# Kernel tuning notes

Hardware: AMD Instinct MI355X
Metric: run time of the kernel (lower is better)

The kernel has to match this reference:

```python
import jax, jax.numpy as jnp
import numpy as np
import math

B, L = 16, 60            # batch, max labels per image
NC, NA = 80, 3           # classes, anchors
NH, NW = 76, 76          # grid
N_CH = 5 + NC
ANCHORS = [1.25, 1.625, 2.0, 3.75, 4.125, 2.875]  # grid units (w,h pairs)
ANCH_MASK = [0, 1, 2]
IGNORE_THRE = 0.5
EPS = 1e-16


def pairwise_iou(a, b, xyxy=True, ciou=False):
    """a: [N,4], b: [M,4] -> [N,M]; mirrors ciou_yolov4 (incl. its xyxy quirks)."""
    if xyxy:
        tl = jnp.maximum(a[:, None, :2], b[None, :, :2])
        br = jnp.minimum(a[:, None, 2:], b[None, :, 2:])
        con_tl = jnp.minimum(a[:, None, :2], b[None, :, :2])
        con_br = jnp.maximum(a[:, None, 2:], b[None, :, 2:])
        rho2 = ((a[:, None, 0] + a[:, None, 2] - b[None, :, 0] - b[None, :, 2]) ** 2
                + (a[:, None, 1] + a[:, None, 3] - b[None, :, 1] - b[None, :, 3]) ** 2) / 4.0
        w1 = a[:, 2] - a[:, 0]; h1 = a[:, 3] - a[:, 1]
        w2 = b[:, 2] - b[:, 0]; h2 = b[:, 3] - b[:, 1]
        area_a = w1 * h1
        area_b = w2 * h2
    else:
        tl = jnp.maximum(a[:, None, :2] - a[:, None, 2:] / 2, b[None, :, :2] - b[None, :, 2:] / 2)
        br = jnp.minimum(a[:, None, :2] + a[:, None, 2:] / 2, b[None, :, :2] + b[None, :, 2:] / 2)
        con_tl = jnp.minimum(a[:, None, :2] - a[:, None, 2:] / 2, b[None, :, :2] - b[None, :, 2:] / 2)
        con_br = jnp.maximum(a[:, None, :2] + a[:, None, 2:] / 2, b[None, :, :2] + b[None, :, 2:] / 2)
        rho2 = (((a[:, None, :2] - b[None, :, :2]) ** 2) / 4.0).sum(-1)
        w1 = a[:, 2]; h1 = a[:, 3]; w2 = b[:, 2]; h2 = b[:, 3]
        area_a = a[:, 2] * a[:, 3]
        area_b = b[:, 2] * b[:, 3]
    en = jnp.prod((tl < br).astype(a.dtype), axis=2)
    area_i = jnp.prod(br - tl, axis=2) * en
    area_u = area_a[:, None] + area_b[None, :] - area_i
    iou = area_i / jnp.maximum(area_u, EPS)  # eps only guards all-zero padded boxes
    if ciou:
        c2 = ((con_br - con_tl) ** 2).sum(-1) + EPS
        v = (4.0 / math.pi ** 2) * (jnp.arctan(w1 / jnp.maximum(h1, EPS))[:, None]
                                    - jnp.arctan(w2 / jnp.maximum(h2, EPS))[None, :]) ** 2
        alpha = jax.lax.stop_gradient(v / jnp.maximum(1.0 - iou + v, EPS))
        return iou - (rho2 / c2 + v * alpha)
    return iou


def _clip_log(x):
    # torch BCE clamps log at -100
    return jnp.maximum(jnp.log(x), -100.0)


def bce_sum(p, t, w=None):
    el = -(t * _clip_log(p) + (1.0 - t) * _clip_log(1.0 - p))
    if w is not None:
        el = el * w
    return el.sum()


def build_targets(pred, labels):
    f32 = pred.dtype
    aw = jnp.asarray(ANCHORS[0:-1:2], f32)  # [NA]
    ah = jnp.asarray(ANCHORS[1::2], f32)
    n_valid = (labels.sum(2) > 0).sum(1)                     # [B]
    valid = jnp.arange(L)[None, :] < n_valid[:, None]        # [B,L]
    tx = labels[:, :, 1] * NW
    ty = labels[:, :, 2] * NH
    tw = labels[:, :, 3] * NW
    th = labels[:, :, 4] * NH
    ti = tx.astype(jnp.int32)  # truncation == floor for positive coords
    tj = ty.astype(jnp.int32)
    # anchor matching: boxes [0,0,w,h] treated as xyxy, CIoU (as in the original)
    ref_anchors = jnp.zeros((NA, 4), f32).at[:, 2].set(aw).at[:, 3].set(ah)
    zeros = jnp.zeros_like(tw)
    tb_wh = jnp.stack([zeros, zeros, tw, th], axis=-1)       # [B,L,4]
    anch_ious = jax.vmap(lambda t: pairwise_iou(t, ref_anchors, xyxy=True, ciou=True))(tb_wh)
    best_n_all = jnp.argmax(anch_ious, axis=-1)              # [B,L]
    best_n = best_n_all % 3
    best_mask = jnp.zeros_like(valid)
    for m in ANCH_MASK:
        best_mask = best_mask | (best_n_all == m)
    sel = valid & best_mask                                  # labels that get assigned
    # ignore mask from pred-vs-truth IoU (xywh, plain IoU)
    tb = jnp.stack([tx, ty, tw, th], axis=-1)                # [B,L,4]
    pious = jax.vmap(lambda p, t: pairwise_iou(p, t, xyxy=False, ciou=False))(
        pred.reshape(B, -1, 4), tb)                          # [B,NA*NH*NW,L]
    pious = jnp.where(valid[:, None, :], pious, -jnp.inf)
    best_iou = pious.max(axis=-1).reshape(B, NA, NH, NW)
    any_sel = sel.any(axis=1)                                # original 'continue' semantics
    obj_mask = jnp.where(any_sel[:, None, None, None],
                         (best_iou <= IGNORE_THRE).astype(f32),
                         jnp.ones((), f32))
    # scatter assignments; a_idx = NA (out of bounds) => dropped
    a_idx = jnp.where(sel, best_n, NA)
    b_idx = jnp.broadcast_to(jnp.arange(B)[:, None], (B, L))
    obj_mask = obj_mask.at[b_idx, a_idx, tj, ti].set(1.0, mode='drop')
    dx = tx - jnp.floor(tx)
    dy = ty - jnp.floor(ty)
    lw = jnp.log(tw / aw[best_n] + EPS)
    lh = jnp.log(th / ah[best_n] + EPS)
    onehot = jax.nn.one_hot(labels[:, :, 0].astype(jnp.int32), NC, dtype=f32)
    tvec = jnp.concatenate([dx[..., None], dy[..., None], lw[..., None], lh[..., None],
                            jnp.ones((B, L, 1), f32), onehot], axis=-1)  # [B,L,N_CH]
    target = jnp.zeros((B, NA, NH, NW, N_CH), f32).at[b_idx, a_idx, tj, ti].set(tvec, mode='drop')
    tgt_mask = jnp.zeros((B, NA, NH, NW, 4 + NC), f32).at[b_idx, a_idx, tj, ti].set(1.0, mode='drop')
    scale = jnp.sqrt(2.0 - tw * th / float(NW * NH))
    tgt_scale = jnp.zeros((B, NA, NH, NW, 2), f32).at[b_idx, a_idx, tj, ti].set(
        jnp.broadcast_to(scale[..., None], (B, L, 2)), mode='drop')
    return obj_mask, tgt_mask, tgt_scale, target


def setup_inputs() -> dict:
    key = jax.random.key(0)
    k1, k2, k3, k4 = jax.random.split(key, 4)
    output = jax.random.normal(k1, (B, NA * N_CH, NH, NW), jnp.float32)
    cls = jax.random.randint(k2, (B, L), 0, NC).astype(jnp.float32)
    xy = jax.random.uniform(k3, (B, L, 2), minval=0.02, maxval=0.98)
    wh = jax.random.uniform(k4, (B, L, 2), minval=0.02, maxval=0.5)
    target = jnp.concatenate([cls[..., None], xy, wh], axis=-1)  # [B,L,5] cls,cx,cy,w,h in [0,1]
    return {"output": output, "target": target}


def reference(output, target):
    labels = jax.lax.stop_gradient(target)
    out = output.reshape(B, NA, N_CH, NH, NW).transpose(0, 1, 3, 4, 2)  # [B,NA,NH,NW,N_CH]
    out = jnp.concatenate([jax.nn.sigmoid(out[..., :2]), out[..., 2:4],
                           jax.nn.sigmoid(out[..., 4:])], axis=-1)
    gx = jnp.arange(NW, dtype=out.dtype)
    gy = jnp.arange(NH, dtype=out.dtype)
    aw = jnp.asarray(ANCHORS[0:-1:2], out.dtype)
    ah = jnp.asarray(ANCHORS[1::2], out.dtype)
    px = out[..., 0] + gx[None, None, None, :]
    py = out[..., 1] + gy[None, None, :, None]
    pw = jnp.exp(out[..., 2]) * aw[None, :, None, None]
    ph = jnp.exp(out[..., 3]) * ah[None, :, None, None]
    pred = jax.lax.stop_gradient(jnp.stack([px, py, pw, ph], axis=-1))  # pred.data in torch
    obj_mask, tgt_mask, tgt_scale, tgt = build_targets(pred, labels)
    oxy = out[..., 0:2] * tgt_mask[..., 0:2]
    owh = out[..., 2:4] * tgt_mask[..., 2:4] * tgt_scale
    oobj = out[..., 4] * obj_mask
    ocls = out[..., 5:] * tgt_mask[..., 4:]
    txy = tgt[..., 0:2] * tgt_mask[..., 0:2]
    twh = tgt[..., 2:4] * tgt_mask[..., 2:4] * tgt_scale
    tobj = tgt[..., 4] * obj_mask
    tcls = tgt[..., 5:] * tgt_mask[..., 4:]
    loss_xy = bce_sum(oxy, txy, w=tgt_scale * tgt_scale)
    loss_wh = ((owh - twh) ** 2).sum() / 2.0
    loss_obj = bce_sum(oobj, tobj)
    loss_cls = bce_sum(ocls, tcls)
    return (loss_xy + loss_wh + loss_obj + loss_cls) / B
```

## Files before the change

### kernel.cpp

```cpp
#include <hip/hip_runtime.h>
#include <math.h>

namespace {

constexpr int kB = 16, kL = 60, kNC = 80, kNA = 3, kNH = 76, kNW = 76, kNCH = 85;
constexpr int kPlane = kNH * kNW;
constexpr int kCellsPerB = kNA * kPlane;
constexpr int kBX = (kCellsPerB + 255) / 256;
constexpr int kNPart = kB * kBX;
constexpr float kEps = 1e-16f;

__device__ float g_partials[kNPart];

__device__ __forceinline__ float sigm(float x) { return 1.0f / (1.0f + expf(-x)); }
__device__ __forceinline__ float softplus(float x) {
  return fmaxf(x, 0.0f) + log1pf(expf(-fabsf(x)));
}
__device__ __forceinline__ float anchW(int a) { return a == 0 ? 1.25f : (a == 1 ? 2.0f : 4.125f); }
__device__ __forceinline__ float anchH(int a) { return a == 0 ? 1.625f : (a == 1 ? 3.75f : 2.875f); }

__global__ __launch_bounds__(256) void main_loss(const float* __restrict__ out,
                                                 const float* __restrict__ labels) {
  const int b = blockIdx.y;
  const int tid = threadIdx.x;
  __shared__ float st[kL][12];
  __shared__ int snv;

  if (tid < 64) {
    const int l = tid;
    const bool in = l < kL;
    float c0 = 0.f, x = 0.f, y = 0.f, w = 0.f, h = 0.f;
    if (in) {
      const float* p = labels + ((size_t)b * kL + l) * 5;
      c0 = p[0]; x = p[1]; y = p[2]; w = p[3]; h = p[4];
    }
    const unsigned long long m = __ballot(in && (c0 + x + y + w + h > 0.0f));
    const int nv = __popcll(m);
    if (l == 0) snv = nv;
    if (in) {
      const bool valid = l < nv;
      const float tx = x * (float)kNW, ty = y * (float)kNH;
      const float tw = w * (float)kNW, th = h * (float)kNH;
      const int ti = (int)tx, tj = (int)ty;

      const float at0 = atanf(tw / fmaxf(th, kEps));
      float best = -INFINITY;
      int bn = 0;
#pragma unroll
      for (int k = 0; k < kNA; ++k) {
        const float aw = anchW(k), ah = anchH(k);
        const float miw = fminf(tw, aw), mih = fminf(th, ah);
        const float en = ((0.0f < miw) && (0.0f < mih)) ? 1.0f : 0.0f;
        const float ai = miw * mih * en;
        const float au = tw * th + aw * ah - ai;
        const float iou = ai / fmaxf(au, kEps);
        const float dw = tw - aw, dh = th - ah;
        const float rho2 = (dw * dw + dh * dh) * 0.25f;
        const float mw = fmaxf(tw, aw), mh = fmaxf(th, ah);
        const float c2 = mw * mw + mh * mh + kEps;
        const float da = at0 - atanf(aw / ah);
        const float v = (4.0f / (float)(M_PI * M_PI)) * da * da;
        const float alpha = v / fmaxf(1.0f - iou + v, kEps);
        const float ciou = iou - (rho2 / c2 + v * alpha);
        if (ciou > best) { best = ciou; bn = k; }
      }
      st[l][0] = tx - tw * 0.5f; st[l][1] = ty - th * 0.5f;
      st[l][2] = tx + tw * 0.5f; st[l][3] = ty + th * 0.5f;
      st[l][4] = tw * th;
      st[l][5] = __int_as_float(valid ? ((bn * kNH + tj) * kNW + ti) : -1);
      st[l][6] = tx - floorf(tx);
      st[l][7] = ty - floorf(ty);
      st[l][8] = logf(tw / anchW(bn) + kEps);
      st[l][9] = logf(th / anchH(bn) + kEps);
      st[l][10] = sqrtf(2.0f - tw * th * (1.0f / (float)(kNW * kNH)));
      st[l][11] = __int_as_float((int)c0);
    }
  }
  __syncthreads();

  float acc = 0.0f;
  const int c = blockIdx.x * 256 + tid;
  int winner = -1;
  if (c < kCellsPerB) {
    const unsigned a = (unsigned)c / (unsigned)kPlane;
    const unsigned r = (unsigned)c - a * (unsigned)kPlane;
    const unsigned j = r / (unsigned)kNW;
    const unsigned i = r - j * (unsigned)kNW;
    const float* base = out + ((size_t)(b * kNA + (int)a) * kNCH) * kPlane + r;
    const float x0 = base[0];
    const float x1 = base[(size_t)kPlane];
    const float x2 = base[(size_t)2 * kPlane];
    const float x3 = base[(size_t)3 * kPlane];
    const float x4 = base[(size_t)4 * kPlane];

    const float px = sigm(x0) + (float)i;
    const float py = sigm(x1) + (float)j;
    const float pw = expf(x2) * anchW((int)a);
    const float ph = expf(x3) * anchH((int)a);
    const float px1 = px - 0.5f * pw, px2 = px + 0.5f * pw;
    const float py1 = py - 0.5f * ph, py2 = py + 0.5f * ph;
    const float ap = pw * ph;

    bool flag = false;
    const int nv = snv;
#pragma unroll 4
    for (int t = 0; t < nv; ++t) {
      const float4 bx = *reinterpret_cast<const float4*>(&st[t][0]);
      const float2 ak = *reinterpret_cast<const float2*>(&st[t][4]);
      const float tlx = fmaxf(px1, bx.x), tly = fmaxf(py1, bx.y);
      const float brx = fminf(px2, bx.z), bry = fminf(py2, bx.w);
      const bool ok = (tlx < brx) && (tly < bry);
      const float ai = ok ? (brx - tlx) * (bry - tly) : 0.0f;
      const float au = ap + ak.x - ai;
      flag = flag || (ai + ai > au);
      if (__float_as_int(ak.y) == c) winner = t;
    }

    const float sp4 = softplus(x4);
    if (winner >= 0) {
      acc += sp4 - x4;
      const float sc = st[winner][10];
      const float w2 = sc * sc;
      acc += (softplus(x0) - st[winner][6] * x0 + softplus(x1) - st[winner][7] * x1) * w2;
      const float d2 = x2 - st[winner][8], d3 = x3 - st[winner][9];
      acc += 0.5f * w2 * (d2 * d2 + d3 * d3);
    } else if (!flag) {
      acc += sp4;
    }
  }

  {
    const int lane = tid & 63;
    unsigned long long pend = __ballot(winner >= 0);
    while (pend) {
      const int src = (int)(__ffsll(pend) - 1);
      pend &= pend - 1;
      const int wc = __shfl(c, src);
      const int wt = __shfl(winner, src);
      const int cls = __float_as_int(st[wt][11]);
      const unsigned wa = (unsigned)wc / (unsigned)kPlane;
      const unsigned wr = (unsigned)wc - wa * (unsigned)kPlane;
      const float* wb = out + ((size_t)(b * kNA + (int)wa) * kNCH + 5) * kPlane + wr;
      const float v0 = wb[(size_t)lane * kPlane];
      float s = softplus(v0) - (lane == cls ? v0 : 0.0f);
      if (lane < kNC - 64) {
        const float v1 = wb[(size_t)(lane + 64) * kPlane];
        s += softplus(v1) - (lane + 64 == cls ? v1 : 0.0f);
      }
#pragma unroll
      for (int off = 32; off > 0; off >>= 1) s += __shfl_down(s, off);
      if (lane == 0) acc += s;
    }
  }

#pragma unroll
  for (int off = 32; off > 0; off >>= 1) acc += __shfl_down(acc, off);
  __shared__ float sred[4];
  if ((tid & 63) == 0) sred[tid >> 6] = acc;
  __syncthreads();
  if (tid == 0) g_partials[b * kBX + blockIdx.x] = sred[0] + sred[1] + sred[2] + sred[3];
}

__global__ void finalize(float* __restrict__ outp) {
  const int tid = threadIdx.x;
  double acc = 0.0;
  for (int idx = tid; idx < kNPart; idx += 256) acc += (double)g_partials[idx];
  __shared__ double s[256];
  s[tid] = acc;
  __syncthreads();
  for (int off = 128; off > 0; off >>= 1) {
    if (tid < off) s[tid] += s[tid + off];
    __syncthreads();
  }
  if (tid == 0) outp[0] = (float)(s[0] / (double)kB);
}

}

extern "C" void kernel_launch(void* const* d_in, const int* in_sizes, int n_in,
                              void* d_out, int out_size, void* d_ws, size_t ws_size,
                              hipStream_t stream) {
  const float* output = (const float*)d_in[0];
  const float* target = (const float*)d_in[1];
  float* outp = (float*)d_out;
  (void)d_ws; (void)ws_size;

  main_loss<<<dim3(kBX, kB), 256, 0, stream>>>(output, target);
  finalize<<<1, 256, 0, stream>>>(outp);
}
```

Measured before the change: 138.6 us.

## Process four cells per thread with float4 loads and shared label loop

Each thread now handles four consecutive grid cells, loading the five head channels as float4 vectors and amortizing each label's shared-memory read across four IoU tests. This cuts the thread count and the LDS traffic in the ignore-mask loop, and widens global loads. In exchange, register pressure rises and there are fewer blocks, which reduces parallelism for this small grid.

New measurement: 153.3 us. 10.6% more time.

```diff
diff --git a/kernel.cpp b/kernel.cpp
--- a/kernel.cpp
+++ b/kernel.cpp
@@ -5,8 +5,9 @@
 
 constexpr int kB = 16, kL = 60, kNC = 80, kNA = 3, kNH = 76, kNW = 76, kNCH = 85;
 constexpr int kPlane = kNH * kNW;
-constexpr int kCellsPerB = kNA * kPlane;
-constexpr int kBX = (kCellsPerB + 255) / 256;
+constexpr int kQuadsPerPlane = kPlane / 4;
+constexpr int kQuadsPerB = kNA * kQuadsPerPlane;
+constexpr int kBX = (kQuadsPerB + 255) / 256;
 constexpr int kNPart = kB * kBX;
 constexpr float kEps = 1e-16f;
 
@@ -42,7 +43,6 @@
       const float tx = x * (float)kNW, ty = y * (float)kNH;
       const float tw = w * (float)kNW, th = h * (float)kNH;
       const int ti = (int)tx, tj = (int)ty;
-
       const float at0 = atanf(tw / fmaxf(th, kEps));
       float best = -INFINITY;
       int bn = 0;
@@ -78,65 +78,80 @@
   }
   __syncthreads();
 
+  const int qid = blockIdx.x * 256 + tid;
+  const bool active = qid < kQuadsPerB;
+  int a = 0, r4 = 0;
+  if (active) { a = qid / kQuadsPerPlane; r4 = (qid - a * kQuadsPerPlane) * 4; }
+  const int cbase = a * kPlane + r4;
+
+  float xc[5][4];
+  float px1[4], px2[4], py1[4], py2[4], ap[4];
+  int winner[4] = {-1, -1, -1, -1};
+  unsigned flags = 0;
   float acc = 0.0f;
-  const int c = blockIdx.x * 256 + tid;
-  int winner = -1;
-  if (c < kCellsPerB) {
-    const unsigned a = (unsigned)c / (unsigned)kPlane;
-    const unsigned r = (unsigned)c - a * (unsigned)kPlane;
-    const unsigned j = r / (unsigned)kNW;
-    const unsigned i = r - j * (unsigned)kNW;
-    const float* base = out + ((size_t)(b * kNA + (int)a) * kNCH) * kPlane + r;
-    const float x0 = base[0];
-    const float x1 = base[(size_t)kPlane];
-    const float x2 = base[(size_t)2 * kPlane];
-    const float x3 = base[(size_t)3 * kPlane];
-    const float x4 = base[(size_t)4 * kPlane];
-
-    const float px = sigm(x0) + (float)i;
-    const float py = sigm(x1) + (float)j;
-    const float pw = expf(x2) * anchW((int)a);
-    const float ph = expf(x3) * anchH((int)a);
-    const float px1 = px - 0.5f * pw, px2 = px + 0.5f * pw;
-    const float py1 = py - 0.5f * ph, py2 = py + 0.5f * ph;
-    const float ap = pw * ph;
-
-    bool flag = false;
+
+  if (active) {
+    const float* base = out + ((size_t)(b * kNA + a) * kNCH) * kPlane + r4;
+#pragma unroll
+    for (int ch = 0; ch < 5; ++ch) {
+      const float4 v = *reinterpret_cast<const float4*>(base + (size_t)ch * kPlane);
+      xc[ch][0] = v.x; xc[ch][1] = v.y; xc[ch][2] = v.z; xc[ch][3] = v.w;
+    }
+    const float aw = anchW(a), ah = anchH(a);
+#pragma unroll
+    for (int k = 0; k < 4; ++k) {
+      const int r = r4 + k;
+      const int j = r / kNW, i = r - j * kNW;
+      const float px = sigm(xc[0][k]) + (float)i;
+      const float py = sigm(xc[1][k]) + (float)j;
+      const float pw = expf(xc[2][k]) * aw;
+      const float ph = expf(xc[3][k]) * ah;
+      px1[k] = px - 0.5f * pw; px2[k] = px + 0.5f * pw;
+      py1[k] = py - 0.5f * ph; py2[k] = py + 0.5f * ph;
+      ap[k] = pw * ph;
+    }
     const int nv = snv;
 #pragma unroll 4
     for (int t = 0; t < nv; ++t) {
       const float4 bx = *reinterpret_cast<const float4*>(&st[t][0]);
       const float2 ak = *reinterpret_cast<const float2*>(&st[t][4]);
-      const float tlx = fmaxf(px1, bx.x), tly = fmaxf(py1, bx.y);
-      const float brx = fminf(px2, bx.z), bry = fminf(py2, bx.w);
-      const bool ok = (tlx < brx) && (tly < bry);
-      const float ai = ok ? (brx - tlx) * (bry - tly) : 0.0f;
-      const float au = ap + ak.x - ai;
-      flag = flag || (ai + ai > au);
-      if (__float_as_int(ak.y) == c) winner = t;
-    }
-
-    const float sp4 = softplus(x4);
-    if (winner >= 0) {
-      acc += sp4 - x4;
-      const float sc = st[winner][10];
-      const float w2 = sc * sc;
-      acc += (softplus(x0) - st[winner][6] * x0 + softplus(x1) - st[winner][7] * x1) * w2;
-      const float d2 = x2 - st[winner][8], d3 = x3 - st[winner][9];
-      acc += 0.5f * w2 * (d2 * d2 + d3 * d3);
-    } else if (!flag) {
-      acc += sp4;
-    }
-  }
-
-  {
-    const int lane = tid & 63;
-    unsigned long long pend = __ballot(winner >= 0);
+      const int key = __float_as_int(ak.y);
+#pragma unroll
+      for (int k = 0; k < 4; ++k) {
+        const float tlx = fmaxf(px1[k], bx.x), tly = fmaxf(py1[k], bx.y);
+        const float brx = fminf(px2[k], bx.z), bry = fminf(py2[k], bx.w);
+        const bool ok = (tlx < brx) && (tly < bry);
+        const float ai = ok ? (brx - tlx) * (bry - tly) : 0.0f;
+        if (ai + ai > ap[k] + ak.x - ai) flags |= (1u << k);
+        if (key == cbase + k) winner[k] = t;
+      }
+    }
+#pragma unroll
+    for (int k = 0; k < 4; ++k) {
+      const float sp4 = softplus(xc[4][k]);
+      if (winner[k] >= 0) {
+        acc += sp4 - xc[4][k];
+        const float sc = st[winner[k]][10];
+        const float w2 = sc * sc;
+        acc += (softplus(xc[0][k]) - st[winner[k]][6] * xc[0][k] +
+                softplus(xc[1][k]) - st[winner[k]][7] * xc[1][k]) * w2;
+        const float d2 = xc[2][k] - st[winner[k]][8], d3 = xc[3][k] - st[winner[k]][9];
+        acc += 0.5f * w2 * (d2 * d2 + d3 * d3);
+      } else if (!((flags >> k) & 1u)) {
+        acc += sp4;
+      }
+    }
+  }
+
+  const int lane = tid & 63;
+#pragma unroll
+  for (int k = 0; k < 4; ++k) {
+    unsigned long long pend = __ballot(winner[k] >= 0);
     while (pend) {
       const int src = (int)(__ffsll(pend) - 1);
       pend &= pend - 1;
-      const int wc = __shfl(c, src);
-      const int wt = __shfl(winner, src);
+      const int wc = __shfl(cbase + k, src);
+      const int wt = __shfl(winner[k], src);
       const int cls = __float_as_int(st[wt][11]);
       const unsigned wa = (unsigned)wc / (unsigned)kPlane;
       const unsigned wr = (unsigned)wc - wa * (unsigned)kPlane;
```

## Precompute per-label target data in a separate kernel and read from global

Applied to the files above, without the earlier changes.

Label preprocessing (best-anchor CIoU selection, box corners, regression targets) moves from every main_loss block into a small prep kernel that runs once per batch image. Results go to global arrays that the main kernel reads through uniform loads. This removes redundant per-block label work and the block-wide barrier before the cell loop, so cell loads can start right away. The cost is an extra kernel launch and global or cache reads of box data in the inner loop instead of LDS reads.

New measurement: 143.1 us. 3.2% more time.

```diff
diff --git a/kernel.cpp b/kernel.cpp
--- a/kernel.cpp
+++ b/kernel.cpp
@@ -10,6 +10,12 @@
 constexpr int kNPart = kB * kBX;
 constexpr float kEps = 1e-16f;
 
+struct __align__(32) BoxT { float x1, y1, x2, y2, area; int key; int p0, p1; };
+struct __align__(32) RegT { float dx, dy, lw, lh, sc; int cls; int p0, p1; };
+
+__device__ BoxT g_boxes[kB][kL];
+__device__ RegT g_regr[kB][kL];
+__device__ int g_nv[kB];
 __device__ float g_partials[kNPart];
 
 __device__ __forceinline__ float sigm(float x) { return 1.0f / (1.0f + expf(-x)); }
@@ -19,110 +25,118 @@
 __device__ __forceinline__ float anchW(int a) { return a == 0 ? 1.25f : (a == 1 ? 2.0f : 4.125f); }
 __device__ __forceinline__ float anchH(int a) { return a == 0 ? 1.625f : (a == 1 ? 3.75f : 2.875f); }
 
+__global__ void prep_labels(const float* __restrict__ labels) {
+  const int b = blockIdx.x;
+  const int l = threadIdx.x;
+  const bool in = l < kL;
+  float c0 = 0.f, x = 0.f, y = 0.f, w = 0.f, h = 0.f;
+  if (in) {
+    const float* p = labels + ((size_t)b * kL + l) * 5;
+    c0 = p[0]; x = p[1]; y = p[2]; w = p[3]; h = p[4];
+  }
+  const unsigned long long m = __ballot(in && (c0 + x + y + w + h > 0.0f));
+  const int nv = __popcll(m);
+  if (l == 0) g_nv[b] = nv;
+  if (!in) return;
+  const bool valid = l < nv;
+
+  const float tx = x * (float)kNW, ty = y * (float)kNH;
+  const float tw = w * (float)kNW, th = h * (float)kNH;
+  const int ti = (int)tx, tj = (int)ty;
+
+  const float at0 = atanf(tw / fmaxf(th, kEps));
+  float best = -INFINITY;
+  int bn = 0;
+#pragma unroll
+  for (int k = 0; k < kNA; ++k) {
+    const float aw = anchW(k), ah = anchH(k);
+    const float miw = fminf(tw, aw), mih = fminf(th, ah);
+    const float en = ((0.0f < miw) && (0.0f < mih)) ? 1.0f : 0.0f;
+    const float ai = miw * mih * en;
+    const float au = tw * th + aw * ah - ai;
+    const float iou = ai / fmaxf(au, kEps);
+    const float dw = tw - aw, dh = th - ah;
+    const float rho2 = (dw * dw + dh * dh) * 0.25f;
+    const float mw = fmaxf(tw, aw), mh = fmaxf(th, ah);
+    const float c2 = mw * mw + mh * mh + kEps;
+    const float da = at0 - atanf(aw / ah);
+    const float v = (4.0f / (float)(M_PI * M_PI)) * da * da;
+    const float alpha = v / fmaxf(1.0f - iou + v, kEps);
+    const float ciou = iou - (rho2 / c2 + v * alpha);
+    if (ciou > best) { best = ciou; bn = k; }
+  }
+
+  BoxT bx;
+  bx.x1 = tx - tw * 0.5f; bx.y1 = ty - th * 0.5f;
+  bx.x2 = tx + tw * 0.5f; bx.y2 = ty + th * 0.5f;
+  bx.area = tw * th;
+  bx.key = valid ? ((bn * kNH + tj) * kNW + ti) : -1;
+  bx.p0 = 0; bx.p1 = 0;
+  g_boxes[b][l] = bx;
+
+  RegT rg;
+  rg.dx = tx - floorf(tx);
+  rg.dy = ty - floorf(ty);
+  rg.lw = logf(tw / anchW(bn) + kEps);
+  rg.lh = logf(th / anchH(bn) + kEps);
+  rg.sc = sqrtf(2.0f - tw * th * (1.0f / (float)(kNW * kNH)));
+  rg.cls = (int)c0;
+  rg.p0 = 0; rg.p1 = 0;
+  g_regr[b][l] = rg;
+}
+
 __global__ __launch_bounds__(256) void main_loss(const float* __restrict__ out,
-                                                 const float* __restrict__ labels) {
+                                                 float* __restrict__ partials_unused) {
   const int b = blockIdx.y;
   const int tid = threadIdx.x;
-  __shared__ float st[kL][12];
-  __shared__ int snv;
-
-  if (tid < 64) {
-    const int l = tid;
-    const bool in = l < kL;
-    float c0 = 0.f, x = 0.f, y = 0.f, w = 0.f, h = 0.f;
-    if (in) {
-      const float* p = labels + ((size_t)b * kL + l) * 5;
-      c0 = p[0]; x = p[1]; y = p[2]; w = p[3]; h = p[4];
-    }
-    const unsigned long long m = __ballot(in && (c0 + x + y + w + h > 0.0f));
-    const int nv = __popcll(m);
-    if (l == 0) snv = nv;
-    if (in) {
-      const bool valid = l < nv;
-      const float tx = x * (float)kNW, ty = y * (float)kNH;
-      const float tw = w * (float)kNW, th = h * (float)kNH;
-      const int ti = (int)tx, tj = (int)ty;
-
-      const float at0 = atanf(tw / fmaxf(th, kEps));
-      float best = -INFINITY;
-      int bn = 0;
-#pragma unroll
-      for (int k = 0; k < kNA; ++k) {
-        const float aw = anchW(k), ah = anchH(k);
-        const float miw = fminf(tw, aw), mih = fminf(th, ah);
-        const float en = ((0.0f < miw) && (0.0f < mih)) ? 1.0f : 0.0f;
-        const float ai = miw * mih * en;
-        const float au = tw * th + aw * ah - ai;
-        const float iou = ai / fmaxf(au, kEps);
-        const float dw = tw - aw, dh = th - ah;
-        const float rho2 = (dw * dw + dh * dh) * 0.25f;
-        const float mw = fmaxf(tw, aw), mh = fmaxf(th, ah);
-        const float c2 = mw * mw + mh * mh + kEps;
-        const float da = at0 - atanf(aw / ah);
-        const float v = (4.0f / (float)(M_PI * M_PI)) * da * da;
-        const float alpha = v / fmaxf(1.0f - iou + v, kEps);
-        const float ciou = iou - (rho2 / c2 + v * alpha);
-        if (ciou > best) { best = ciou; bn = k; }
-      }
-      st[l][0] = tx - tw * 0.5f; st[l][1] = ty - th * 0.5f;
-      st[l][2] = tx + tw * 0.5f; st[l][3] = ty + th * 0.5f;
-      st[l][4] = tw * th;
-      st[l][5] = __int_as_float(valid ? ((bn * kNH + tj) * kNW + ti) : -1);
-      st[l][6] = tx - floorf(tx);
-      st[l][7] = ty - floorf(ty);
-      st[l][8] = logf(tw / anchW(bn) + kEps);
-      st[l][9] = logf(th / anchH(bn) + kEps);
-      st[l][10] = sqrtf(2.0f - tw * th * (1.0f / (float)(kNW * kNH)));
-      st[l][11] = __int_as_float((int)c0);
-    }
-  }
-  __syncthreads();
+  const int c = blockIdx.x * 256 + tid;
+  const bool active = c < kCellsPerB;
+  const int cs = active ? c : 0;
+  const int ckey = active ? c : -9;
+
+  const unsigned a = (unsigned)cs / (unsigned)kPlane;
+  const unsigned r = (unsigned)cs - a * (unsigned)kPlane;
+  const unsigned j = r / (unsigned)kNW;
+  const unsigned i = r - j * (unsigned)kNW;
+  const float* base = out + ((size_t)(b * kNA + (int)a) * kNCH) * kPlane + r;
+  const float x0 = base[0];
+  const float x1 = base[(size_t)kPlane];
+  const float x2 = base[(size_t)2 * kPlane];
+  const float x3 = base[(size_t)3 * kPlane];
+  const float x4 = base[(size_t)4 * kPlane];
+
+  const float px = sigm(x0) + (float)i;
+  const float py = sigm(x1) + (float)j;
+  const float pw = expf(x2) * anchW((int)a);
+  const float ph = expf(x3) * anchH((int)a);
+  const float px1 = px - 0.5f * pw, px2 = px + 0.5f * pw;
+  const float py1 = py - 0.5f * ph, py2 = py + 0.5f * ph;
+  const float ap = pw * ph;
+
+  bool flag = false;
+  int winner = -1;
+  const int nv = g_nv[b];
+  const BoxT* __restrict__ bp = g_boxes[b];
+#pragma unroll 4
+  for (int t = 0; t < nv; ++t) {
+    const BoxT bx = bp[t];
+    const float tlx = fmaxf(px1, bx.x1), tly = fmaxf(py1, bx.y1);
+    const float brx = fminf(px2, bx.x2), bry = fminf(py2, bx.y2);
+    const bool ok = (tlx < brx) && (tly < bry);
+    const float ai = ok ? (brx - tlx) * (bry - tly) : 0.0f;
+    flag = flag || (ai + ai > ap + bx.area - ai);
+    if (bx.key == ckey) winner = t;
+  }
 
   float acc = 0.0f;
-  const int c = blockIdx.x * 256 + tid;
-  int winner = -1;
-  if (c < kCellsPerB) {
-    const unsigned a = (unsigned)c / (unsigned)kPlane;
-    const unsigned r = (unsigned)c - a * (unsigned)kPlane;
-    const unsigned j = r / (unsigned)kNW;
-    const unsigned i = r - j * (unsigned)kNW;
-    const float* base = out + ((size_t)(b * kNA + (int)a) * kNCH) * kPlane + r;
-    const float x0 = base[0];
-    const float x1 = base[(size_t)kPlane];
-    const float x2 = base[(size_t)2 * kPlane];
-    const float x3 = base[(size_t)3 * kPlane];
-    const float x4 = base[(size_t)4 * kPlane];
-
-    const float px = sigm(x0) + (float)i;
-    const float py = sigm(x1) + (float)j;
-    const float pw = expf(x2) * anchW((int)a);
-    const float ph = expf(x3) * anchH((int)a);
-    const float px1 = px - 0.5f * pw, px2 = px + 0.5f * pw;
-    const float py1 = py - 0.5f * ph, py2 = py + 0.5f * ph;
-    const float ap = pw * ph;
-
-    bool flag = false;
-    const int nv = snv;
-#pragma unroll 4
-    for (int t = 0; t < nv; ++t) {
-      const float4 bx = *reinterpret_cast<const float4*>(&st[t][0]);
-      const float2 ak = *reinterpret_cast<const float2*>(&st[t][4]);
-      const float tlx = fmaxf(px1, bx.x), tly = fmaxf(py1, bx.y);
-      const float brx = fminf(px2, bx.z), bry = fminf(py2, bx.w);
-      const bool ok = (tlx < brx) && (tly < bry);
-      const float ai = ok ? (brx - tlx) * (bry - tly) : 0.0f;
-      const float au = ap + ak.x - ai;
-      flag = flag || (ai + ai > au);
-      if (__float_as_int(ak.y) == c) winner = t;
-    }
-
+  if (active) {
     const float sp4 = softplus(x4);
     if (winner >= 0) {
+      const RegT rg = g_regr[b][winner];
       acc += sp4 - x4;
-      const float sc = st[winner][10];
-      const float w2 = sc * sc;
-      acc += (softplus(x0) - st[winner][6] * x0 + softplus(x1) - st[winner][7] * x1) * w2;
-      const float d2 = x2 - st[winner][8], d3 = x3 - st[winner][9];
+      const float w2 = rg.sc * rg.sc;
+      acc += (softplus(x0) - rg.dx * x0 + softplus(x1) - rg.dy * x1) * w2;
+      const float d2 = x2 - rg.lw, d3 = x3 - rg.lh;
       acc += 0.5f * w2 * (d2 * d2 + d3 * d3);
     } else if (!flag) {
       acc += sp4;
@@ -137,7 +151,7 @@
       pend &= pend - 1;
       const int wc = __shfl(c, src);
       const int wt = __shfl(winner, src);
-      const int cls = __float_as_int(st[wt][11]);
+      const int cls = g_regr[b][wt].cls;
       const unsigned wa = (unsigned)wc / (unsigned)kPlane;
       const unsigned wr = (unsigned)wc - wa * (unsigned)kPlane;
       const float* wb = out + ((size_t)(b * kNA + (int)wa) * kNCH + 5) * kPlane + wr;
@@ -185,6 +199,7 @@
   float* outp = (float*)d_out;
   (void)d_ws; (void)ws_size;
 
-  main_loss<<<dim3(kBX, kB), 256, 0, stream>>>(output, target);
+  prep_labels<<<kB, 64, 0, stream>>>(target);
+  main_loss<<<dim3(kBX, kB), 256, 0, stream>>>(output, nullptr);
   finalize<<<1, 256, 0, stream>>>(outp);
 }
```

## Fuse finalize into main kernel via last-block ticket and precompute winners in LDS

Applied to the files above, without the earlier changes.

Drops the separate finalize kernel. Each block publishes its partial sum and bumps a global ticket, and the last block to arrive does the double-precision reduction and resets the ticket. Winner cells are now found by scattering label keys into a per-block shared array with atomicMax, which takes the per-cell key compare out of the IoU loop. This saves one kernel launch and some inner-loop work, at the cost of atomics and an extra block barrier.

Measured after the change: 194.8 us. 1.41x slower.

```diff
diff --git a/kernel.cpp b/kernel.cpp
--- a/kernel.cpp
+++ b/kernel.cpp
@@ -11,6 +11,7 @@
 constexpr float kEps = 1e-16f;
 
 __device__ float g_partials[kNPart];
+__device__ unsigned g_ticket = 0;
 
 __device__ __forceinline__ float sigm(float x) { return 1.0f / (1.0f + expf(-x)); }
 __device__ __forceinline__ float softplus(float x) {
@@ -19,13 +20,20 @@
 __device__ __forceinline__ float anchW(int a) { return a == 0 ? 1.25f : (a == 1 ? 2.0f : 4.125f); }
 __device__ __forceinline__ float anchH(int a) { return a == 0 ? 1.625f : (a == 1 ? 3.75f : 2.875f); }
 
-__global__ __launch_bounds__(256) void main_loss(const float* __restrict__ out,
-                                                 const float* __restrict__ labels) {
+__global__ __launch_bounds__(256) void yolo_loss(const float* __restrict__ out,
+                                                 const float* __restrict__ labels,
+                                                 float* __restrict__ outp) {
   const int b = blockIdx.y;
   const int tid = threadIdx.x;
+  const int cb0 = blockIdx.x * 256;
   __shared__ float st[kL][12];
+  __shared__ int swin[256];
   __shared__ int snv;
-
+  __shared__ int sLast;
+
+  swin[tid] = -1;
+
+  int mykey = -1;
   if (tid < 64) {
     const int l = tid;
     const bool in = l < kL;
@@ -42,7 +50,6 @@
       const float tx = x * (float)kNW, ty = y * (float)kNH;
       const float tw = w * (float)kNW, th = h * (float)kNH;
       const int ti = (int)tx, tj = (int)ty;
-
       const float at0 = atanf(tw / fmaxf(th, kEps));
       float best = -INFINITY;
       int bn = 0;
@@ -67,55 +74,61 @@
       st[l][0] = tx - tw * 0.5f; st[l][1] = ty - th * 0.5f;
       st[l][2] = tx + tw * 0.5f; st[l][3] = ty + th * 0.5f;
       st[l][4] = tw * th;
-      st[l][5] = __int_as_float(valid ? ((bn * kNH + tj) * kNW + ti) : -1);
       st[l][6] = tx - floorf(tx);
       st[l][7] = ty - floorf(ty);
       st[l][8] = logf(tw / anchW(bn) + kEps);
       st[l][9] = logf(th / anchH(bn) + kEps);
       st[l][10] = sqrtf(2.0f - tw * th * (1.0f / (float)(kNW * kNH)));
       st[l][11] = __int_as_float((int)c0);
-    }
-  }
-  __syncthreads();
+      mykey = valid ? ((bn * kNH + tj) * kNW + ti) : -1;
+    }
+  }
+  __syncthreads();
+
+  if (tid < kL && mykey >= cb0 && mykey < cb0 + 256) {
+    atomicMax(&swin[mykey - cb0], tid);
+  }
+  __syncthreads();
+
+  const int c = cb0 + tid;
+  const bool active = c < kCellsPerB;
+  const int cs = active ? c : 0;
+  const int winner = active ? swin[tid] : -1;
+
+  const unsigned a = (unsigned)cs / (unsigned)kPlane;
+  const unsigned r = (unsigned)cs - a * (unsigned)kPlane;
+  const unsigned j = r / (unsigned)kNW;
+  const unsigned i = r - j * (unsigned)kNW;
+  const float* base = out + ((size_t)(b * kNA + (int)a) * kNCH) * kPlane + r;
+  const float x0 = base[0];
+  const float x1 = base[(size_t)kPlane];
+  const float x2 = base[(size_t)2 * kPlane];
+  const float x3 = base[(size_t)3 * kPlane];
+  const float x4 = base[(size_t)4 * kPlane];
+
+  const float px = sigm(x0) + (float)i;
+  const float py = sigm(x1) + (float)j;
+  const float pw = expf(x2) * anchW((int)a);
+  const float ph = expf(x3) * anchH((int)a);
+  const float px1 = px - 0.5f * pw, px2 = px + 0.5f * pw;
+  const float py1 = py - 0.5f * ph, py2 = py + 0.5f * ph;
+  const float ap = pw * ph;
+
+  bool flag = false;
+  const int nv = snv;
+#pragma unroll 4
+  for (int t = 0; t < nv; ++t) {
+    const float4 bx = *reinterpret_cast<const float4*>(&st[t][0]);
+    const float areaT = st[t][4];
+    const float tlx = fmaxf(px1, bx.x), tly = fmaxf(py1, bx.y);
+    const float brx = fminf(px2, bx.z), bry = fminf(py2, bx.w);
+    const bool ok = (tlx < brx) && (tly < bry);
+    const float ai = ok ? (brx - tlx) * (bry - tly) : 0.0f;
+    flag = flag || (ai + ai > ap + areaT - ai);
+  }
 
   float acc = 0.0f;
-  const int c = blockIdx.x * 256 + tid;
-  int winner = -1;
-  if (c < kCellsPerB) {
-    const unsigned a = (unsigned)c / (unsigned)kPlane;
-    const unsigned r = (unsigned)c - a * (unsigned)kPlane;
-    const unsigned j = r / (unsigned)kNW;
-    const unsigned i = r - j * (unsigned)kNW;
-    const float* base = out + ((size_t)(b * kNA + (int)a) * kNCH) * kPlane + r;
-    const float x0 = base[0];
-    const float x1 = base[(size_t)kPlane];
-    const float x2 = base[(size_t)2 * kPlane];
-    const float x3 = base[(size_t)3 * kPlane];
-    const float x4 = base[(size_t)4 * kPlane];
-
-    const float px = sigm(x0) + (float)i;
-    const float py = sigm(x1) + (float)j;
-    const float pw = expf(x2) * anchW((int)a);
-    const float ph = expf(x3) * anchH((int)a);
-    const float px1 = px - 0.5f * pw, px2 = px + 0.5f * pw;
-    const float py1 = py - 0.5f * ph, py2 = py + 0.5f * ph;
-    const float ap = pw * ph;
-
-    bool flag = false;
-    const int nv = snv;
-#pragma unroll 4
-    for (int t = 0; t < nv; ++t) {
-      const float4 bx = *reinterpret_cast<const float4*>(&st[t][0]);
-      const float2 ak = *reinterpret_cast<const float2*>(&st[t][4]);
-      const float tlx = fmaxf(px1, bx.x), tly = fmaxf(py1, bx.y);
-      const float brx = fminf(px2, bx.z), bry = fminf(py2, bx.w);
-      const bool ok = (tlx < brx) && (tly < bry);
-      const float ai = ok ? (brx - tlx) * (bry - tly) : 0.0f;
-      const float au = ap + ak.x - ai;
-      flag = flag || (ai + ai > au);
-      if (__float_as_int(ak.y) == c) winner = t;
-    }
-
+  if (active) {
     const float sp4 = softplus(x4);
     if (winner >= 0) {
       acc += sp4 - x4;
@@ -158,21 +171,36 @@
   __shared__ float sred[4];
   if ((tid & 63) == 0) sred[tid >> 6] = acc;
   __syncthreads();
-  if (tid == 0) g_partials[b * kBX + blockIdx.x] = sred[0] + sred[1] + sred[2] + sred[3];
-}
-
-__global__ void finalize(float* __restrict__ outp) {
-  const int tid = threadIdx.x;
-  double acc = 0.0;
-  for (int idx = tid; idx < kNPart; idx += 256) acc += (double)g_partials[idx];
-  __shared__ double s[256];
-  s[tid] = acc;
-  __syncthreads();
-  for (int off = 128; off > 0; off >>= 1) {
-    if (tid < off) s[tid] += s[tid + off];
+
+  const int pid = b * kBX + blockIdx.x;
+  if (tid == 0) {
+    const float part = sred[0] + sred[1] + sred[2] + sred[3];
+    __hip_atomic_store(&g_partials[pid], part, __ATOMIC_RELEASE, __HIP_MEMORY_SCOPE_AGENT);
+    const unsigned t = __hip_atomic_fetch_add(&g_ticket, 1u, __ATOMIC_ACQ_REL,
+                                              __HIP_MEMORY_SCOPE_AGENT);
+    sLast = (t == (unsigned)(kNPart - 1)) ? 1 : 0;
+  }
+  __syncthreads();
+
+  if (sLast) {
+    double dacc = 0.0;
+    for (int idx = tid; idx < kNPart; idx += 256) {
+      const float pv = __hip_atomic_load(&g_partials[idx], __ATOMIC_ACQUIRE,
+                                         __HIP_MEMORY_SCOPE_AGENT);
+      dacc += (double)pv;
+    }
+    __shared__ double sd[256];
+    sd[tid] = dacc;
     __syncthreads();
-  }
-  if (tid == 0) outp[0] = (float)(s[0] / (double)kB);
+    for (int off = 128; off > 0; off >>= 1) {
+      if (tid < off) sd[tid] += sd[tid + off];
+      __syncthreads();
+    }
+    if (tid == 0) {
+      outp[0] = (float)(sd[0] / (double)kB);
+      __hip_atomic_store(&g_ticket, 0u, __ATOMIC_RELEASE, __HIP_MEMORY_SCOPE_AGENT);
+    }
+  }
 }
 
 }
@@ -185,6 +213,5 @@
   float* outp = (float*)d_out;
   (void)d_ws; (void)ws_size;
 
-  main_loss<<<dim3(kBX, kB), 256, 0, stream>>>(output, target);
-  finalize<<<1, 256, 0, stream>>>(outp);
-}
+  yolo_loss<<<dim3(kBX, kB), 256, 0, stream>>>(output, target, outp);
+}
```
